# Optimization experiments

Hardware: AMD Instinct MI355X
Metric: run time of the kernel (lower is better)

## Reference

```python
import jax, jax.numpy as jnp
import numpy as np

# dims mirroring the torch module: dim=32 (MVN), omega=8, d_head=n_embd//n_head
B, T, E, DH = 8, 2048, 1024, 32
OMEGA, DIM = 8, 32
M = OMEGA * DIM  # 256 random features (omega concatenated N(0, I_dim) samples)


def setup_inputs() -> dict:
    key = jax.random.key(0)
    ks = jax.random.split(key, 8)
    s = 1.0 / np.sqrt(E).astype(np.float32)  # torch Linear-like init scale
    return {
        "x": jax.random.normal(ks[0], (B, T, E), jnp.float32),
        "Wq": jax.random.normal(ks[1], (E, DH), jnp.float32) * s,
        "bq": jax.random.normal(ks[2], (DH,), jnp.float32) * s,
        "Wk": jax.random.normal(ks[3], (E, DH), jnp.float32) * s,
        "bk": jax.random.normal(ks[4], (DH,), jnp.float32) * s,
        "Wv": jax.random.normal(ks[5], (E, DH), jnp.float32) * s,
        "bv": jax.random.normal(ks[6], (DH,), jnp.float32) * s,
        # random-feature matrix: omega stacked samples from N(0, I_DIM) -> [M, DH]
        "w": jax.random.normal(ks[7], (M, DH), jnp.float32),
    }


def reference(x, Wq, bq, Wk, bk, Wv, bv, w):
    # projections (as in Head.forward)
    q = x @ Wq + bq  # [B,T,DH]
    k = x @ Wk + bk  # [B,T,DH]
    v = x @ Wv + bv  # computed but unused, exactly as in the source
    del v
    # Aprox_softmax (FAVOR+-style hyperbolic random features), vectorized per token
    z = k + q                                          # [B,T,DH]
    zsqr = jnp.sum(k * k, -1) + jnp.sum(q * q, -1)     # [B,T]  (per-token norms)
    A = jnp.exp(-0.5 * zsqr)                           # [B,T]
    cosH = jnp.cosh(jnp.einsum('btd,md->btm', z, w))   # [B,T,M]
    R = A[..., None] * cosH                            # [B,T,M]
    return R
```

## Files before the change

### kernel.cpp

```cpp
#include <hip/hip_runtime.h>
#include <cstdint>

#define E_DIM   1024
#define DH      32
#define M_FEAT  256
#define BT      16384

typedef __attribute__((ext_vector_type(8))) _Float16 f16x8;
typedef __attribute__((ext_vector_type(4))) float f32x4;


__device__ __forceinline__ unsigned packh2(_Float16 a, _Float16 b) {
    union { _Float16 h[2]; unsigned u; } t;
    t.h[0] = a; t.h[1] = b;
    return t.u;
}

__device__ __forceinline__ void splitf16_2(float f0, float f1, unsigned& ph, unsigned& pl) {
    _Float16 h0 = (_Float16)f0, h1 = (_Float16)f1;
    float l0 = f0 - (float)h0, l1 = f1 - (float)h1;
    ph = packh2(h0, h1);
    pl = packh2((_Float16)l0, (_Float16)l1);
}

__device__ __forceinline__ void splitf16_8(const float4& a, const float4& b,
                                           uint4& uh, uint4& ul) {
    splitf16_2(a.x, a.y, uh.x, ul.x);
    splitf16_2(a.z, a.w, uh.y, ul.y);
    splitf16_2(b.x, b.y, uh.z, ul.z);
    splitf16_2(b.z, b.w, uh.w, ul.w);
}

__global__ __launch_bounds__(256) void k_prep(
    const float* __restrict__ Wq, const float* __restrict__ Wk,
    short* __restrict__ ws)
{
    const int gid  = blockIdx.x * 256 + threadIdx.x;
    const int j0   = (gid & 1) * 4;
    const int lane = (gid >> 1) & 63;
    const int sub  = (gid >> 7) & 31;
    const int nt   = gid >> 12;
    const int n_g  = nt * 16 + (lane & 15);
    const int k_g  = sub * 32 + (lane >> 4) * 8 + j0;
    const float* __restrict__ src = (n_g < 32) ? Wq : Wk;
    const int col = n_g & 31;
    float f0 = src[(size_t)(k_g + 0) * DH + col];
    float f1 = src[(size_t)(k_g + 1) * DH + col];
    float f2 = src[(size_t)(k_g + 2) * DH + col];
    float f3 = src[(size_t)(k_g + 3) * DH + col];
    uint2 ph;
    ph.x = packh2((_Float16)f0, (_Float16)f1);
    ph.y = packh2((_Float16)f2, (_Float16)f3);
    *(uint2*)(ws + (size_t)gid * 4) = ph;
}

#define TB 32
#define XS2 136
#define QS 68

__global__ __launch_bounds__(256, 3) void k_main(
    const float* __restrict__ x, const float* __restrict__ bq,
    const float* __restrict__ bk, const short* __restrict__ ws,
    const float* __restrict__ w, float* __restrict__ out)
{
    __shared__ __align__(16) short xh_s[2][TB * XS2];
    __shared__ __align__(16) short xl_s[2][TB * XS2];
    __shared__ __align__(16) float qk_f[TB * QS];

    const int tid  = threadIdx.x;
    const int lane = tid & 63;
    const int wv   = __builtin_amdgcn_readfirstlane(tid >> 6);
    const int ln15 = lane & 15;
    const int g    = lane >> 4;
    const long t0  = (long)blockIdx.x * TB;

    const int nrow = wv * 16 + ln15;
    const float bias = (nrow < 32) ? bq[nrow] : bk[nrow - 32];

    const int kq = tid & 15;
    const int mr = tid >> 4;

    f32x4 acc0 = {0.f, 0.f, 0.f, 0.f};
    f32x4 acc1 = {0.f, 0.f, 0.f, 0.f};

    const short* wpB = ws + (size_t)(wv * 32) * 512 + lane * 8;
    const float* xr0 = x + (t0 + mr) * (size_t)E_DIM + kq * 8;
    const float* xr1 = x + (t0 + mr + 16) * (size_t)E_DIM + kq * 8;

    float4 s0[4], s1[4];
    {
        float4 t0v = *(const float4*)(xr0 + 0), t1v = *(const float4*)(xr0 + 4);
        float4 t2v = *(const float4*)(xr1 + 0), t3v = *(const float4*)(xr1 + 4);
        s1[0] = *(const float4*)(xr0 + 128);
        s1[1] = *(const float4*)(xr0 + 132);
        s1[2] = *(const float4*)(xr1 + 128);
        s1[3] = *(const float4*)(xr1 + 132);
        uint4 uh, ul;
        splitf16_8(t0v, t1v, uh, ul);
        *(uint4*)&xh_s[0][mr * XS2 + kq * 8] = uh;
        *(uint4*)&xl_s[0][mr * XS2 + kq * 8] = ul;
        splitf16_8(t2v, t3v, uh, ul);
        *(uint4*)&xh_s[0][(mr + 16) * XS2 + kq * 8] = uh;
        *(uint4*)&xl_s[0][(mr + 16) * XS2 + kq * 8] = ul;
    }

#pragma unroll
    for (int p = 0; p < 8; ++p) {
        __syncthreads();
        if (p < 6) {
            float4* d = (p & 1) ? s1 : s0;
            d[0] = *(const float4*)(xr0 + (p + 2) * 128);
            d[1] = *(const float4*)(xr0 + (p + 2) * 128 + 4);
            d[2] = *(const float4*)(xr1 + (p + 2) * 128);
            d[3] = *(const float4*)(xr1 + (p + 2) * 128 + 4);
        }
        f16x8 bfr[4];
#pragma unroll
        for (int j = 0; j < 4; ++j)
            bfr[j] = *(const f16x8*)(wpB + (size_t)(p * 4 + j) * 512);
#pragma unroll
        for (int j = 0; j < 4; ++j) {
            f16x8 ah0 = *(const f16x8*)&xh_s[p & 1][ln15 * XS2 + j * 32 + g * 8];
            f16x8 al0 = *(const f16x8*)&xl_s[p & 1][ln15 * XS2 + j * 32 + g * 8];
            f16x8 ah1 = *(const f16x8*)&xh_s[p & 1][(ln15 + 16) * XS2 + j * 32 + g * 8];
            f16x8 al1 = *(const f16x8*)&xl_s[p & 1][(ln15 + 16) * XS2 + j * 32 + g * 8];
            acc0 = __builtin_amdgcn_mfma_f32_16x16x32_f16(ah0, bfr[j], acc0, 0, 0, 0);
            acc0 = __builtin_amdgcn_mfma_f32_16x16x32_f16(al0, bfr[j], acc0, 0, 0, 0);
            acc1 = __builtin_amdgcn_mfma_f32_16x16x32_f16(ah1, bfr[j], acc1, 0, 0, 0);
            acc1 = __builtin_amdgcn_mfma_f32_16x16x32_f16(al1, bfr[j], acc1, 0, 0, 0);
        }
        if (p < 7) {
            const float4* s = ((p + 1) & 1) ? s1 : s0;
            uint4 uh, ul;
            splitf16_8(s[0], s[1], uh, ul);
            *(uint4*)&xh_s[(p + 1) & 1][mr * XS2 + kq * 8] = uh;
            *(uint4*)&xl_s[(p + 1) & 1][mr * XS2 + kq * 8] = ul;
            splitf16_8(s[2], s[3], uh, ul);
            *(uint4*)&xh_s[(p + 1) & 1][(mr + 16) * XS2 + kq * 8] = uh;
            *(uint4*)&xl_s[(p + 1) & 1][(mr + 16) * XS2 + kq * 8] = ul;
        }
    }

    float4 wfa[4], wfb[4];
#pragma unroll
    for (int i = 0; i < 4; ++i) {
        const int nf = (wv * 4 + i) * 16 + ln15;
        wfa[i] = *(const float4*)(w + (size_t)nf * DH + g * 8);
        wfb[i] = *(const float4*)(w + (size_t)nf * DH + g * 8 + 4);
    }

#pragma unroll
    for (int r = 0; r < 4; ++r) {
        qk_f[(g * 4 + r) * QS + nrow]        = acc0[r] + bias;
        qk_f[(16 + g * 4 + r) * QS + nrow]   = acc1[r] + bias;
    }
    __syncthreads();

    const float LOG2E = 1.4426950408889634f;
    f16x8 a_h[2], a_l[2];
    float pwv[2];
#pragma unroll
    for (int mt = 0; mt < 2; ++mt) {
        const int row = mt * 16 + ln15;
        float4 qlo = *(const float4*)&qk_f[row * QS + g * 8];
        float4 qhi = *(const float4*)&qk_f[row * QS + g * 8 + 4];
        float4 klo = *(const float4*)&qk_f[row * QS + 32 + g * 8];
        float4 khi = *(const float4*)&qk_f[row * QS + 32 + g * 8 + 4];
        float4 zlo = {qlo.x + klo.x, qlo.y + klo.y, qlo.z + klo.z, qlo.w + klo.w};
        float4 zhi = {qhi.x + khi.x, qhi.y + khi.y, qhi.z + khi.z, qhi.w + khi.w};
        uint4 uh, ul;
        splitf16_8(zlo, zhi, uh, ul);
        a_h[mt] = __builtin_bit_cast(f16x8, uh);
        a_l[mt] = __builtin_bit_cast(f16x8, ul);
        float pw = qlo.x*qlo.x + qlo.y*qlo.y + qlo.z*qlo.z + qlo.w*qlo.w
                 + qhi.x*qhi.x + qhi.y*qhi.y + qhi.z*qhi.z + qhi.w*qhi.w
                 + klo.x*klo.x + klo.y*klo.y + klo.z*klo.z + klo.w*klo.w
                 + khi.x*khi.x + khi.y*khi.y + khi.z*khi.z + khi.w*khi.w;
        pw += __shfl_xor(pw, 16);
        pw += __shfl_xor(pw, 32);
        pwv[mt] = pw;
    }
    float lnAv[2][4];
#pragma unroll
    for (int mt = 0; mt < 2; ++mt)
#pragma unroll
        for (int r = 0; r < 4; ++r)
            lnAv[mt][r] = -0.5f * LOG2E * __shfl(pwv[mt], g * 4 + r);

    f32x4 facc[4][2];
#pragma unroll
    for (int i = 0; i < 4; ++i)
#pragma unroll
        for (int mt = 0; mt < 2; ++mt) facc[i][mt] = (f32x4){0.f,0.f,0.f,0.f};

#pragma unroll
    for (int i = 0; i < 4; ++i) {
        uint4 uw;
        uw.x = packh2((_Float16)wfa[i].x, (_Float16)wfa[i].y);
        uw.y = packh2((_Float16)wfa[i].z, (_Float16)wfa[i].w);
        uw.z = packh2((_Float16)wfb[i].x, (_Float16)wfb[i].y);
        uw.w = packh2((_Float16)wfb[i].z, (_Float16)wfb[i].w);
        f16x8 w8 = __builtin_bit_cast(f16x8, uw);
#pragma unroll
        for (int mt = 0; mt < 2; ++mt) {
            facc[i][mt] = __builtin_amdgcn_mfma_f32_16x16x32_f16(a_h[mt], w8, facc[i][mt], 0, 0, 0);
            facc[i][mt] = __builtin_amdgcn_mfma_f32_16x16x32_f16(a_l[mt], w8, facc[i][mt], 0, 0, 0);
        }
    }

#pragma unroll
    for (int i = 0; i < 4; ++i) {
        const int n = (wv * 4 + i) * 16 + ln15;
#pragma unroll
        for (int mt = 0; mt < 2; ++mt) {
#pragma unroll
            for (int r = 0; r < 4; ++r) {
                float s = facc[i][mt][r] * LOG2E;
                float R = 0.5f * (__builtin_amdgcn_exp2f(lnAv[mt][r] + s)
                                + __builtin_amdgcn_exp2f(lnAv[mt][r] - s));
                __builtin_nontemporal_store(R, &out[(t0 + mt * 16 + g * 4 + r) * M_FEAT + n]);
            }
        }
    }
}

extern "C" void kernel_launch(void* const* d_in, const int* in_sizes, int n_in,
                              void* d_out, int out_size, void* d_ws, size_t ws_size,
                              hipStream_t stream) {
    const float* x  = (const float*)d_in[0];
    const float* Wq = (const float*)d_in[1];
    const float* bq = (const float*)d_in[2];
    const float* Wk = (const float*)d_in[3];
    const float* bk = (const float*)d_in[4];
    const float* w  = (const float*)d_in[7];
    float* out = (float*)d_out;
    short* ws  = (short*)d_ws;

    k_prep<<<dim3(64), dim3(256), 0, stream>>>(Wq, Wk, ws);
    k_main<<<dim3(BT / TB), dim3(256), 0, stream>>>(x, bq, bk, ws, w, out);
}
```

Measured before the change: 118.9 us.

## Stream x tiles with async global-to-LDS loads and triple buffering

Replaces the register-staged fp32 loads plus fp16 hi/lo split stores into LDS with direct global_load_lds async copies of raw fp32 x into a triple-buffered, XOR-swizzled LDS tile. The hi/lo split now happens after reading LDS in the MFMA loop. Weight fragments are double-buffered in registers, and waits use explicit vmcnt and s_barrier. The aim is to hide global latency and cut VGPR staging, but each wave now redoes the split, LDS use grows (occupancy bound lowered to 2), and the hand-counted vmcnt must stay correct.

```diff
diff --git a/kernel.cpp b/kernel.cpp
--- a/kernel.cpp
+++ b/kernel.cpp
@@ -30,6 +30,10 @@
     splitf16_2(b.x, b.y, uh.z, ul.z);
     splitf16_2(b.z, b.w, uh.w, ul.w);
 }
+
+#define ASYNC16(gp, lp) __builtin_amdgcn_global_load_lds(                      \
+    (const __attribute__((address_space(1))) unsigned int*)(gp),               \
+    (__attribute__((address_space(3))) unsigned int*)(lp), 16, 0, 0)
 
 __global__ __launch_bounds__(256) void k_prep(
     const float* __restrict__ Wq, const float* __restrict__ Wk,
@@ -55,16 +59,14 @@
 }
 
 #define TB 32
-#define XS2 136
 #define QS 68
 
-__global__ __launch_bounds__(256, 3) void k_main(
+__global__ __launch_bounds__(256, 2) void k_main(
     const float* __restrict__ x, const float* __restrict__ bq,
     const float* __restrict__ bk, const short* __restrict__ ws,
     const float* __restrict__ w, float* __restrict__ out)
 {
-    __shared__ __align__(16) short xh_s[2][TB * XS2];
-    __shared__ __align__(16) short xl_s[2][TB * XS2];
+    __shared__ __align__(16) float x_s[3][TB * 128];
     __shared__ __align__(16) float qk_f[TB * QS];
 
     const int tid  = threadIdx.x;
@@ -77,67 +79,68 @@
     const int nrow = wv * 16 + ln15;
     const float bias = (nrow < 32) ? bq[nrow] : bk[nrow - 32];
 
-    const int kq = tid & 15;
-    const int mr = tid >> 4;
+    const float* gsrc[4];
+#pragma unroll
+    for (int i = 0; i < 4; ++i) {
+        const int G   = i * 256 + tid;
+        const int row = G >> 5, gd = G & 31;
+        gsrc[i] = x + (t0 + row) * (size_t)E_DIM + (gd ^ (row & 7)) * 4;
+    }
+    const short* wpB = ws + (size_t)(wv * 32) * 512 + lane * 8;
+    const int sw = ln15 & 7;
 
     f32x4 acc0 = {0.f, 0.f, 0.f, 0.f};
     f32x4 acc1 = {0.f, 0.f, 0.f, 0.f};
-
-    const short* wpB = ws + (size_t)(wv * 32) * 512 + lane * 8;
-    const float* xr0 = x + (t0 + mr) * (size_t)E_DIM + kq * 8;
-    const float* xr1 = x + (t0 + mr + 16) * (size_t)E_DIM + kq * 8;
-
-    float4 s0[4], s1[4];
-    {
-        float4 t0v = *(const float4*)(xr0 + 0), t1v = *(const float4*)(xr0 + 4);
-        float4 t2v = *(const float4*)(xr1 + 0), t3v = *(const float4*)(xr1 + 4);
-        s1[0] = *(const float4*)(xr0 + 128);
-        s1[1] = *(const float4*)(xr0 + 132);
-        s1[2] = *(const float4*)(xr1 + 128);
-        s1[3] = *(const float4*)(xr1 + 132);
-        uint4 uh, ul;
-        splitf16_8(t0v, t1v, uh, ul);
-        *(uint4*)&xh_s[0][mr * XS2 + kq * 8] = uh;
-        *(uint4*)&xl_s[0][mr * XS2 + kq * 8] = ul;
-        splitf16_8(t2v, t3v, uh, ul);
-        *(uint4*)&xh_s[0][(mr + 16) * XS2 + kq * 8] = uh;
-        *(uint4*)&xl_s[0][(mr + 16) * XS2 + kq * 8] = ul;
-    }
+    f16x8 bfr[2][4];
+
+#pragma unroll
+    for (int i = 0; i < 4; ++i) ASYNC16(gsrc[i], &x_s[0][i * 1024 + wv * 256]);
+#pragma unroll
+    for (int i = 0; i < 4; ++i) ASYNC16(gsrc[i] + 128, &x_s[1][i * 1024 + wv * 256]);
+    __builtin_amdgcn_sched_barrier(0);
+#pragma unroll
+    for (int j = 0; j < 4; ++j)
+        bfr[0][j] = *(const f16x8*)(wpB + (size_t)j * 512);
+    __syncthreads();
 
 #pragma unroll
     for (int p = 0; p < 8; ++p) {
-        __syncthreads();
         if (p < 6) {
-            float4* d = (p & 1) ? s1 : s0;
-            d[0] = *(const float4*)(xr0 + (p + 2) * 128);
-            d[1] = *(const float4*)(xr0 + (p + 2) * 128 + 4);
-            d[2] = *(const float4*)(xr1 + (p + 2) * 128);
-            d[3] = *(const float4*)(xr1 + (p + 2) * 128 + 4);
-        }
-        f16x8 bfr[4];
-#pragma unroll
-        for (int j = 0; j < 4; ++j)
-            bfr[j] = *(const f16x8*)(wpB + (size_t)(p * 4 + j) * 512);
+#pragma unroll
+            for (int i = 0; i < 4; ++i)
+                ASYNC16(gsrc[i] + (p + 2) * 128, &x_s[(p + 2) % 3][i * 1024 + wv * 256]);
+        }
+        __builtin_amdgcn_sched_barrier(0);
+        if (p < 7) {
+#pragma unroll
+            for (int j = 0; j < 4; ++j)
+                bfr[(p + 1) & 1][j] = *(const f16x8*)(wpB + (size_t)((p + 1) * 4 + j) * 512);
+        }
+        __builtin_amdgcn_sched_barrier(0);
+        const char* xb = (const char*)x_s[p % 3];
 #pragma unroll
         for (int j = 0; j < 4; ++j) {
-            f16x8 ah0 = *(const f16x8*)&xh_s[p & 1][ln15 * XS2 + j * 32 + g * 8];
-            f16x8 al0 = *(const f16x8*)&xl_s[p & 1][ln15 * XS2 + j * 32 + g * 8];
-            f16x8 ah1 = *(const f16x8*)&xh_s[p & 1][(ln15 + 16) * XS2 + j * 32 + g * 8];
-            f16x8 al1 = *(const f16x8*)&xl_s[p & 1][(ln15 + 16) * XS2 + j * 32 + g * 8];
-            acc0 = __builtin_amdgcn_mfma_f32_16x16x32_f16(ah0, bfr[j], acc0, 0, 0, 0);
-            acc0 = __builtin_amdgcn_mfma_f32_16x16x32_f16(al0, bfr[j], acc0, 0, 0, 0);
-            acc1 = __builtin_amdgcn_mfma_f32_16x16x32_f16(ah1, bfr[j], acc1, 0, 0, 0);
-            acc1 = __builtin_amdgcn_mfma_f32_16x16x32_f16(al1, bfr[j], acc1, 0, 0, 0);
+            const int qa = j * 8 + g * 2;
+            float4 fa0 = *(const float4*)(xb + ln15 * 512        + ((qa ^ sw) << 4));
+            float4 fb0 = *(const float4*)(xb + ln15 * 512        + (((qa + 1) ^ sw) << 4));
+            float4 fa1 = *(const float4*)(xb + (ln15 + 16) * 512 + ((qa ^ sw) << 4));
+            float4 fb1 = *(const float4*)(xb + (ln15 + 16) * 512 + (((qa + 1) ^ sw) << 4));
+            uint4 uh, ul;
+            splitf16_8(fa0, fb0, uh, ul);
+            f16x8 ah0 = __builtin_bit_cast(f16x8, uh);
+            f16x8 al0 = __builtin_bit_cast(f16x8, ul);
+            splitf16_8(fa1, fb1, uh, ul);
+            f16x8 ah1 = __builtin_bit_cast(f16x8, uh);
+            f16x8 al1 = __builtin_bit_cast(f16x8, ul);
+            acc0 = __builtin_amdgcn_mfma_f32_16x16x32_f16(ah0, bfr[p & 1][j], acc0, 0, 0, 0);
+            acc0 = __builtin_amdgcn_mfma_f32_16x16x32_f16(al0, bfr[p & 1][j], acc0, 0, 0, 0);
+            acc1 = __builtin_amdgcn_mfma_f32_16x16x32_f16(ah1, bfr[p & 1][j], acc1, 0, 0, 0);
+            acc1 = __builtin_amdgcn_mfma_f32_16x16x32_f16(al1, bfr[p & 1][j], acc1, 0, 0, 0);
         }
         if (p < 7) {
-            const float4* s = ((p + 1) & 1) ? s1 : s0;
-            uint4 uh, ul;
-            splitf16_8(s[0], s[1], uh, ul);
-            *(uint4*)&xh_s[(p + 1) & 1][mr * XS2 + kq * 8] = uh;
-            *(uint4*)&xl_s[(p + 1) & 1][mr * XS2 + kq * 8] = ul;
-            splitf16_8(s[2], s[3], uh, ul);
-            *(uint4*)&xh_s[(p + 1) & 1][(mr + 16) * XS2 + kq * 8] = uh;
-            *(uint4*)&xl_s[(p + 1) & 1][(mr + 16) * XS2 + kq * 8] = ul;
+            asm volatile("s_waitcnt vmcnt(8)" ::: "memory");
+            __builtin_amdgcn_s_barrier();
+            __builtin_amdgcn_sched_barrier(0);
         }
     }
 
```

Measured after the change: 121.3 us. 2.0% more time.
